# Kernel tuning notes

Hardware: AMD Instinct MI355X
Metric: run time of the kernel (lower is better)

The kernel has to match this reference:

```python
import jax, jax.numpy as jnp
import numpy as np

N_NODES = 100000
N_EDGES = 1600000
N_GRAPHS = 1024
IN_G, HID_G = 64, 128
IN_T, H1, H2 = 200, 256, 128
CONCAT = 2 * HID_G + H2  # 384


def setup_inputs() -> dict:
    key = jax.random.key(0)
    ks = jax.random.split(key, 24)
    def lin(k, fin, fout):
        kw, kb = jax.random.split(k)
        s = 1.0 / np.sqrt(fin)
        return (jax.random.uniform(kw, (fin, fout), jnp.float32, -s, s),
                jax.random.uniform(kb, (fout,), jnp.float32, -s, s))
    Wg1, bg1 = lin(ks[0], IN_G, HID_G)
    Wg2, bg2 = lin(ks[1], HID_G, HID_G)
    Wg3, bg3 = lin(ks[2], HID_G, HID_G)
    Wg4, bg4 = lin(ks[3], HID_G, HID_G)
    Wt1, bt1 = lin(ks[4], IN_T, H1)
    Wt2, bt2 = lin(ks[5], H1, H2)
    Wf1, bf1 = lin(ks[6], CONCAT, H1)
    Wf2, bf2 = lin(ks[7], H1, H2)
    Wf3, bf3 = lin(ks[8], H2, 1)
    x_graph = jax.random.normal(ks[9], (N_NODES, IN_G), jnp.float32)
    edge_index = jax.random.randint(ks[10], (2, N_EDGES), 0, N_NODES, jnp.int32)
    batch = jnp.sort(jax.random.randint(ks[11], (N_NODES,), 0, N_GRAPHS, jnp.int32))
    x_tabular = jax.random.normal(ks[12], (N_GRAPHS, IN_T), jnp.float32)
    return {"x_graph": x_graph, "edge_index": edge_index, "batch": batch,
            "x_tabular": x_tabular,
            "Wg1": Wg1, "bg1": bg1, "Wg2": Wg2, "bg2": bg2,
            "Wg3": Wg3, "bg3": bg3, "Wg4": Wg4, "bg4": bg4,
            "Wt1": Wt1, "bt1": bt1, "Wt2": Wt2, "bt2": bt2,
            "Wf1": Wf1, "bf1": bf1, "Wf2": Wf2, "bf2": bf2,
            "Wf3": Wf3, "bf3": bf3}


def _gcn(x, src, dst, norm, W, b, n):
    # x' = D^-1/2 A_hat D^-1/2 (x W) + b, scatter-add over edges
    h = x @ W
    msg = h[src] * norm[:, None]
    return jax.ops.segment_sum(msg, dst, num_segments=n) + b


def reference(x_graph, edge_index, batch, x_tabular,
              Wg1, bg1, Wg2, bg2, Wg3, bg3, Wg4, bg4,
              Wt1, bt1, Wt2, bt2, Wf1, bf1, Wf2, bf2, Wf3, bf3):
    n = x_graph.shape[0]
    b = x_tabular.shape[0]
    ar = jnp.arange(n, dtype=edge_index.dtype)
    # self-loops added once in Multi_Modal.forward + once inside GCNConv (default)
    src = jnp.concatenate([edge_index[0], ar, ar])
    dst = jnp.concatenate([edge_index[1], ar, ar])
    deg = jax.ops.segment_sum(jnp.ones(src.shape, x_graph.dtype), dst, num_segments=n)
    dinv = jnp.where(deg > 0, jax.lax.rsqrt(deg), 0.0)
    norm = dinv[src] * dinv[dst]
    h = jax.nn.relu(_gcn(x_graph, src, dst, norm, Wg1, bg1, n))
    h = jax.nn.relu(_gcn(h, src, dst, norm, Wg2, bg2, n))
    h = jax.nn.relu(_gcn(h, src, dst, norm, Wg3, bg3, n))
    h = jax.nn.relu(_gcn(h, src, dst, norm, Wg4, bg4, n))
    # global mean/max pool per graph
    cnt = jax.ops.segment_sum(jnp.ones((n,), h.dtype), batch, num_segments=b)
    mean = jax.ops.segment_sum(h, batch, num_segments=b) / jnp.maximum(cnt, 1.0)[:, None]
    mx = jax.ops.segment_max(h, batch, num_segments=b)
    x1 = jnp.concatenate([mean, mx], axis=1)
    # tabular branch
    x2 = jax.nn.relu(jax.nn.relu(x_tabular @ Wt1 + bt1) @ Wt2 + bt2)
    # fused head
    x = jnp.concatenate([x1, x2], axis=1)
    x = jax.nn.relu(x @ Wf1 + bf1)
    x = jax.nn.relu(x @ Wf2 + bf2)
    return jax.nn.sigmoid(x @ Wf3 + bf3)
```

## Files before the change

### kernel.cpp

```cpp
#include <hip/hip_runtime.h>
#include <hip/hip_bf16.h>
#include <math.h>

#define N_NODES  100000
#define N_EDGES  1600000
#define N_GRAPHS 1024

typedef __hip_bfloat16 bf16;
typedef unsigned short u16;
typedef unsigned int   u32;
typedef __attribute__((ext_vector_type(8))) short bf8_t;
typedef __attribute__((ext_vector_type(4))) float f4_t;

__device__ __forceinline__ float b2f(bf16 v) { return __bfloat162float(v); }
__device__ __forceinline__ u16 bfbits(float f) {
    bf16 h = __float2bfloat16(f);
    return *reinterpret_cast<u16*>(&h);
}
__device__ __forceinline__ float lo_bf(u32 u) { return __uint_as_float(u << 16); }
__device__ __forceinline__ float hi_bf(u32 u) { return __uint_as_float(u & 0xffff0000u); }

__global__ void sniff_init(const u16* __restrict__ xg, int* __restrict__ flag,
                           int* __restrict__ degi) {
    int i = blockIdx.x * 256 + threadIdx.x;
    if (i < N_NODES) degi[i] = 2;
    if (blockIdx.x == 0 && threadIdx.x == 0) {
        int bad = 0;
        for (int k = 0; k < 256; ++k) {
            float f = __uint_as_float(((u32)xg[k]) << 16);
            if (!(fabsf(f) < 100.f)) bad++;
        }
        *flag = (bad == 0) ? 1 : 0;
    }
}

#define NT 19
struct WTask { const void* src; void* dst; int n; int mode; };
struct PrepArgs { WTask t[NT]; int bstart[NT]; };

__global__ void prep_k(PrepArgs args, const int* __restrict__ flag) {
    int b = blockIdx.x, ti = 0;
    while (ti < NT - 1 && b >= args.bstart[ti + 1]) ++ti;
    int idx = (b - args.bstart[ti]) * 256 + threadIdx.x;
    WTask tk = args.t[ti];
    if (idx >= tk.n) return;
    int isb = *flag;
    if (tk.mode == 0) {
        float v = isb ? b2f(((const bf16*)tk.src)[idx]) : ((const float*)tk.src)[idx];
        ((float*)tk.dst)[idx] = v;
    } else if (tk.mode == 1) {
        int bseg = idx >> 9, r = idx & 511;
        int L = r >> 3, j = r & 7;
        int kb = bseg >> 3, tt = bseg & 7;
        int k = kb * 32 + ((L >> 4) << 3) + j;
        int n = (tt << 4) + (L & 15);
        int so = k * 128 + n;
        float v = isb ? b2f(((const bf16*)tk.src)[so]) : ((const float*)tk.src)[so];
        ((u16*)tk.dst)[idx] = bfbits(v);
    } else {
        u16 v = isb ? ((const u16*)tk.src)[idx] : bfbits(((const float*)tk.src)[idx]);
        ((u16*)tk.dst)[idx] = v;
    }
}

__global__ void deg_edges(const int* __restrict__ dst, int* __restrict__ degi) {
    int e = blockIdx.x * blockDim.x + threadIdx.x;
    if (e < N_EDGES) atomicAdd(&degi[dst[e]], 1);
}

#define SCAN_B 256
__global__ void scan1(const int* __restrict__ degi, int* __restrict__ ex,
                      int* __restrict__ bsum, float* __restrict__ dinv) {
    __shared__ int s[SCAN_B];
    int i = blockIdx.x * SCAN_B + threadIdx.x;
    int dg = (i < N_NODES) ? degi[i] : 2;
    int v = dg - 2;
    s[threadIdx.x] = v;
    __syncthreads();
    for (int off = 1; off < SCAN_B; off <<= 1) {
        int t = (threadIdx.x >= off) ? s[threadIdx.x - off] : 0;
        __syncthreads();
        if (threadIdx.x >= off) s[threadIdx.x] += t;
        __syncthreads();
    }
    if (i < N_NODES) {
        ex[i] = s[threadIdx.x] - v;
        dinv[i] = rsqrtf((float)dg);
    }
    if (threadIdx.x == SCAN_B - 1) bsum[blockIdx.x] = s[SCAN_B - 1];
}

__global__ void scan2(int* __restrict__ bsum, int nb) {
    __shared__ int s[512];
    int i = threadIdx.x;
    int v = (i < nb) ? bsum[i] : 0;
    s[i] = v;
    __syncthreads();
    for (int off = 1; off < 512; off <<= 1) {
        int t = (i >= off) ? s[i - off] : 0;
        __syncthreads();
        if (i >= off) s[i] += t;
        __syncthreads();
    }
    if (i < nb) bsum[i] = s[i] - v;
}

__global__ void scan3(int* __restrict__ rowptr, const int* __restrict__ bsum,
                      int* __restrict__ cnt) {
    int i = blockIdx.x * SCAN_B + threadIdx.x;
    if (i >= N_NODES) return;
    rowptr[i] += bsum[blockIdx.x];
    cnt[i] = 0;
}

__global__ void fill_csr(const int* __restrict__ src, const int* __restrict__ dst,
                         const float* __restrict__ dinv, const int* __restrict__ rowptr,
                         int* __restrict__ cnt, u32* __restrict__ csr4) {
    int e = blockIdx.x * 256 + threadIdx.x;
    if (e >= N_EDGES) return;
    int s = src[e], d = dst[e];
    int pos = rowptr[d] + atomicAdd(&cnt[d], 1);
    u32 q = (u32)__float2int_rn(dinv[s] * 32767.f);
    csr4[pos] = (q << 17) | (u32)s;
}

template<int K, bool EPI>
__global__ __launch_bounds__(256) void gemm_mfma(const u16* __restrict__ A,
        const u16* __restrict__ Wm, const float* __restrict__ bias,
        u16* __restrict__ Out, int M)
{
    int wave = threadIdx.x >> 6, lane = threadIdx.x & 63;
    int rowBase = blockIdx.x * 64 + wave * 16;
    int quad = lane >> 4, low = lane & 15;
    int arow = rowBase + low;
    if (arow >= M) arow = M - 1;
    const u16* ap = A + (size_t)arow * K + quad * 8;

    f4_t acc[8];
#pragma unroll
    for (int t = 0; t < 8; ++t) acc[t] = (f4_t)(0.f);

#pragma unroll
    for (int kb = 0; kb < K / 32; ++kb) {
        bf8_t a = *(const bf8_t*)(ap + kb * 32);
#pragma unroll
        for (int t = 0; t < 8; ++t) {
            bf8_t b = *(const bf8_t*)(Wm + (((kb << 3) + t) << 9) + lane * 8);
            acc[t] = __builtin_amdgcn_mfma_f32_16x16x32_bf16(a, b, acc[t], 0, 0, 0);
        }
    }

    int orow0 = rowBase + quad * 4;
#pragma unroll
    for (int t = 0; t < 8; ++t) {
        float bn = EPI ? bias[t * 16 + low] : 0.f;
#pragma unroll
        for (int j = 0; j < 4; ++j) {
            int r = orow0 + j;
            float v = acc[t][j];
            if (EPI) v = fmaxf(v + bn, 0.f);
            if (r < M) Out[(size_t)r * 128 + t * 16 + low] = bfbits(v);
        }
    }
}

__global__ __launch_bounds__(256) void gather_agg(
        const int* __restrict__ rowptr, const int* __restrict__ cnt,
        const u32* __restrict__ csr4, const u16* __restrict__ H,
        const float* __restrict__ dinv, const float* __restrict__ bias,
        u16* __restrict__ A)
{
    int node = blockIdx.x * 4 + (threadIdx.x >> 6);
    if (node >= N_NODES) return;
    int lane = threadIdx.x & 63;
    const u32* H2 = (const u32*)H;
    float2 bb = ((const float2*)bias)[lane];
    float dv = dinv[node];
    u32 h0 = H2[(size_t)node * 64 + lane];
    float accx = 2.f * dv * lo_bf(h0);
    float accy = 2.f * dv * hi_bf(h0);
    int p = rowptr[node];
    int end = p + cnt[node];
    const float qs = 1.f / 32767.f;
    for (; p + 8 <= end; p += 8) {
        u32 m0 = csr4[p],     m1 = csr4[p + 1];
        u32 m2 = csr4[p + 2], m3 = csr4[p + 3];
        u32 m4 = csr4[p + 4], m5 = csr4[p + 5];
        u32 m6 = csr4[p + 6], m7 = csr4[p + 7];
        u32 v0 = H2[(size_t)(m0 & 0x1FFFFu) * 64 + lane];
        u32 v1 = H2[(size_t)(m1 & 0x1FFFFu) * 64 + lane];
        u32 v2 = H2[(size_t)(m2 & 0x1FFFFu) * 64 + lane];
        u32 v3 = H2[(size_t)(m3 & 0x1FFFFu) * 64 + lane];
        u32 v4 = H2[(size_t)(m4 & 0x1FFFFu) * 64 + lane];
        u32 v5 = H2[(size_t)(m5 & 0x1FFFFu) * 64 + lane];
        u32 v6 = H2[(size_t)(m6 & 0x1FFFFu) * 64 + lane];
        u32 v7 = H2[(size_t)(m7 & 0x1FFFFu) * 64 + lane];
        float w0 = (float)(m0 >> 17) * qs, w1 = (float)(m1 >> 17) * qs;
        float w2 = (float)(m2 >> 17) * qs, w3 = (float)(m3 >> 17) * qs;
        float w4 = (float)(m4 >> 17) * qs, w5 = (float)(m5 >> 17) * qs;
        float w6 = (float)(m6 >> 17) * qs, w7 = (float)(m7 >> 17) * qs;
        accx += w0 * lo_bf(v0) + w1 * lo_bf(v1) + w2 * lo_bf(v2) + w3 * lo_bf(v3)
              + w4 * lo_bf(v4) + w5 * lo_bf(v5) + w6 * lo_bf(v6) + w7 * lo_bf(v7);
        accy += w0 * hi_bf(v0) + w1 * hi_bf(v1) + w2 * hi_bf(v2) + w3 * hi_bf(v3)
              + w4 * hi_bf(v4) + w5 * hi_bf(v5) + w6 * hi_bf(v6) + w7 * hi_bf(v7);
    }
    for (; p < end; ++p) {
        u32 m = csr4[p];
        u32 v = H2[(size_t)(m & 0x1FFFFu) * 64 + lane];
        float w = (float)(m >> 17) * qs;
        accx += w * lo_bf(v); accy += w * hi_bf(v);
    }
    accx = fmaxf(accx * dv + bb.x, 0.f);
    accy = fmaxf(accy * dv + bb.y, 0.f);
    u32 pack = ((u32)bfbits(accy) << 16) | (u32)bfbits(accx);
    ((u32*)A)[(size_t)node * 64 + lane] = pack;
}

__global__ __launch_bounds__(256) void gather_x(
        const int* __restrict__ rowptr, const int* __restrict__ cnt,
        const u32* __restrict__ csr4, const u16* __restrict__ X,
        const float* __restrict__ dinv, u16* __restrict__ G)
{
    int node = blockIdx.x * 4 + (threadIdx.x >> 6);
    if (node >= N_NODES) return;
    int lane = threadIdx.x & 63;
    int half = lane >> 5, fi = lane & 31;
    const u32* X2 = (const u32*)X;
    float dv = dinv[node];
    float accx = 0.f, accy = 0.f;
    if (half == 0) {
        u32 h0 = X2[(size_t)node * 32 + fi];
        accx = 2.f * dv * lo_bf(h0); accy = 2.f * dv * hi_bf(h0);
    }
    int rp = rowptr[node];
    int end = rp + cnt[node];
    const float qs = 1.f / 32767.f;
    int p = rp + half;
    for (; p + 6 < end; p += 8) {
        u32 m0 = csr4[p],     m1 = csr4[p + 2];
        u32 m2 = csr4[p + 4], m3 = csr4[p + 6];
        u32 v0 = X2[(size_t)(m0 & 0x1FFFFu) * 32 + fi];
        u32 v1 = X2[(size_t)(m1 & 0x1FFFFu) * 32 + fi];
        u32 v2 = X2[(size_t)(m2 & 0x1FFFFu) * 32 + fi];
        u32 v3 = X2[(size_t)(m3 & 0x1FFFFu) * 32 + fi];
        float w0 = (float)(m0 >> 17) * qs, w1 = (float)(m1 >> 17) * qs;
        float w2 = (float)(m2 >> 17) * qs, w3 = (float)(m3 >> 17) * qs;
        accx += w0 * lo_bf(v0) + w1 * lo_bf(v1) + w2 * lo_bf(v2) + w3 * lo_bf(v3);
        accy += w0 * hi_bf(v0) + w1 * hi_bf(v1) + w2 * hi_bf(v2) + w3 * hi_bf(v3);
    }
    for (; p < end; p += 2) {
        u32 m = csr4[p];
        u32 v = X2[(size_t)(m & 0x1FFFFu) * 32 + fi];
        float w = (float)(m >> 17) * qs;
        accx += w * lo_bf(v); accy += w * hi_bf(v);
    }
    accx += __shfl_xor(accx, 32);
    accy += __shfl_xor(accy, 32);
    if (half == 0) {
        accx *= dv; accy *= dv;
        u32 pack = ((u32)bfbits(accy) << 16) | (u32)bfbits(accx);
        ((u32*)G)[(size_t)node * 32 + fi] = pack;
    }
}

__global__ __launch_bounds__(256) void tail_k(const u16* __restrict__ A,
        const int* __restrict__ batch, const void* __restrict__ x_tab,
        const float* __restrict__ Wt1, const float* __restrict__ bt1,
        const float* __restrict__ Wt2, const float* __restrict__ bt2,
        const float* __restrict__ Wf1, const float* __restrict__ bf1,
        const float* __restrict__ Wf2, const float* __restrict__ bf2,
        const float* __restrict__ Wf3, const float* __restrict__ bf3,
        void* __restrict__ out, const int* __restrict__ flagp)
{
    __shared__ float xs[384];
    __shared__ float t1s[256];
    __shared__ float u1s[256];
    __shared__ float u2s[128];
    __shared__ float xts[200];
    __shared__ float ps[256], pm[256];
    __shared__ int sb[2];
    int g = blockIdx.x;
    int tid = threadIdx.x;
    if (tid == 0) {
        int lo = 0, hi = N_NODES;
        while (lo < hi) { int m = (lo + hi) >> 1; if (batch[m] < g) lo = m + 1; else hi = m; }
        sb[0] = lo;
        hi = N_NODES;
        while (lo < hi) { int m = (lo + hi) >> 1; if (batch[m] < g + 1) lo = m + 1; else hi = m; }
        sb[1] = lo;
    }
    int isb = *flagp;
    if (tid < 200)
        xts[tid] = isb ? b2f(((const bf16*)x_tab)[(size_t)g * 200 + tid])
                       : ((const float*)x_tab)[(size_t)g * 200 + tid];
    __syncthreads();
    int start = sb[0], end = sb[1];
    int t = tid & 127, half = tid >> 7;
    float sum = 0.f, mx = -3.4e38f;
    for (int n = start + half; n < end; n += 2) {
        float v = __uint_as_float(((u32)A[(size_t)n * 128 + t]) << 16);
        sum += v; mx = fmaxf(mx, v);
    }
    ps[tid] = sum; pm[tid] = mx;
    __syncthreads();
    if (half == 0) {
        int c = end - start;
        float s2 = ps[t] + ps[t + 128];
        float m2 = fmaxf(pm[t], pm[t + 128]);
        xs[t] = s2 / (float)(c > 0 ? c : 1);
        xs[128 + t] = (c > 0) ? m2 : 0.f;
    }
    float acc = bt1[tid];
    for (int k = 0; k < 200; ++k) acc += xts[k] * Wt1[k * 256 + tid];
    t1s[tid] = fmaxf(acc, 0.f);
    __syncthreads();
    if (tid < 128) {
        acc = bt2[tid];
        for (int k = 0; k < 256; ++k) acc += t1s[k] * Wt2[k * 128 + tid];
        xs[256 + tid] = fmaxf(acc, 0.f);
    }
    __syncthreads();
    acc = bf1[tid];
    for (int k = 0; k < 384; ++k) acc += xs[k] * Wf1[k * 256 + tid];
    u1s[tid] = fmaxf(acc, 0.f);
    __syncthreads();
    if (tid < 128) {
        acc = bf2[tid];
        for (int k = 0; k < 256; ++k) acc += u1s[k] * Wf2[k * 128 + tid];
        u2s[tid] = fmaxf(acc, 0.f);
    }
    __syncthreads();
    if (tid < 64) {
        float a = u2s[tid] * Wf3[tid] + u2s[tid + 64] * Wf3[tid + 64];
        for (int off = 32; off > 0; off >>= 1) a += __shfl_down(a, off);
        if (tid == 0) {
            float z = a + bf3[0];
            float sg = 1.f / (1.f + expf(-z));
            if (isb) ((bf16*)out)[g] = __float2bfloat16(sg);
            else     ((float*)out)[g] = sg;
        }
    }
}

extern "C" void kernel_launch(void* const* d_in, const int* in_sizes, int n_in,
                              void* d_out, int out_size, void* d_ws, size_t ws_size,
                              hipStream_t stream) {
    const void* x_graph    = d_in[0];
    const int*  edge_index = (const int*)d_in[1];
    const int*  batch      = (const int*)d_in[2];
    const void* x_tab      = d_in[3];

    const int* src  = edge_index;
    const int* dstp = edge_index + N_EDGES;

    char* wsp = (char*)d_ws;
    int*  flag = (int*)wsp;                      wsp += 16;
    u16*  A16  = (u16*)wsp;                      wsp += (size_t)N_NODES * 128 * 2;
    u16*  B16  = (u16*)wsp;                      wsp += (size_t)N_NODES * 128 * 2;
    u16*  X16  = (u16*)wsp;                      wsp += (size_t)N_NODES * 64 * 2;
    u16*  G16  = (u16*)wsp;                      wsp += (size_t)N_NODES * 64 * 2;
    u16*  Wm[4];
    Wm[0] = (u16*)wsp;                           wsp += 64 * 128 * 2;
    Wm[1] = (u16*)wsp;                           wsp += 128 * 128 * 2;
    Wm[2] = (u16*)wsp;                           wsp += 128 * 128 * 2;
    Wm[3] = (u16*)wsp;                           wsp += 128 * 128 * 2;
    float* p = (float*)wsp;
    float* bg1f = p; p += 128;
    float* bg2f = p; p += 128;
    float* bg3f = p; p += 128;
    float* bg4f = p; p += 128;
    float* Wt1f = p; p += 200 * 256; float* bt1f = p; p += 256;
    float* Wt2f = p; p += 256 * 128; float* bt2f = p; p += 128;
    float* Wf1f = p; p += 384 * 256; float* bf1f = p; p += 256;
    float* Wf2f = p; p += 256 * 128; float* bf2f = p; p += 128;
    float* Wf3f = p; p += 128;       float* bf3f = p; p += 4;
    int*   degi   = (int*)p;            p += N_NODES;
    float* dinv   = p;                  p += N_NODES;
    int*   rowptr = (int*)p;            p += N_NODES;
    int*   cnt    = (int*)p;            p += N_NODES;
    int*   bsum   = (int*)p;            p += 512;
    u32*   csr4   = (u32*)p;            p += N_EDGES;

    sniff_init<<<(N_NODES + 255) / 256, 256, 0, stream>>>((const u16*)x_graph, flag, degi);

    PrepArgs pa;
    auto setT = [&](int i, const void* s, void* d, int n, int mode) {
        pa.t[i].src = s; pa.t[i].dst = d; pa.t[i].n = n; pa.t[i].mode = mode;
    };
    setT(0,  d_in[4],  Wm[0], 64 * 128, 1);
    setT(1,  d_in[6],  Wm[1], 128 * 128, 1);
    setT(2,  d_in[8],  Wm[2], 128 * 128, 1);
    setT(3,  d_in[10], Wm[3], 128 * 128, 1);
    setT(4,  d_in[12], Wt1f, 200 * 256, 0);
    setT(5,  d_in[14], Wt2f, 256 * 128, 0);
    setT(6,  d_in[16], Wf1f, 384 * 256, 0);
    setT(7,  d_in[18], Wf2f, 256 * 128, 0);
    setT(8,  d_in[20], Wf3f, 128, 0);
    setT(9,  d_in[5],  bg1f, 128, 0);
    setT(10, d_in[7],  bg2f, 128, 0);
    setT(11, d_in[9],  bg3f, 128, 0);
    setT(12, d_in[11], bg4f, 128, 0);
    setT(13, d_in[13], bt1f, 256, 0);
    setT(14, d_in[15], bt2f, 128, 0);
    setT(15, d_in[17], bf1f, 256, 0);
    setT(16, d_in[19], bf2f, 128, 0);
    setT(17, d_in[21], bf3f, 1, 0);
    setT(18, d_in[0],  X16, N_NODES * 64, 2);
    int totalBlocks = 0;
    for (int i = 0; i < NT; ++i) {
        pa.bstart[i] = totalBlocks;
        totalBlocks += (pa.t[i].n + 255) / 256;
    }
    prep_k<<<totalBlocks, 256, 0, stream>>>(pa, flag);

    const int nb = (N_NODES + SCAN_B - 1) / SCAN_B;
    deg_edges<<<(N_EDGES + 255) / 256, 256, 0, stream>>>(dstp, degi);
    scan1<<<nb, SCAN_B, 0, stream>>>(degi, rowptr, bsum, dinv);
    scan2<<<1, 512, 0, stream>>>(bsum, nb);
    scan3<<<nb, SCAN_B, 0, stream>>>(rowptr, bsum, cnt);
    fill_csr<<<(N_EDGES + 255) / 256, 256, 0, stream>>>(src, dstp, dinv, rowptr, cnt, csr4);

    const int gemmGrid = (N_NODES + 63) / 64;
    const int aggGrid  = (N_NODES + 3) / 4;

    gather_x<<<aggGrid, 256, 0, stream>>>(rowptr, cnt, csr4, X16, dinv, G16);
    gemm_mfma<64, true><<<gemmGrid, 256, 0, stream>>>(G16, Wm[0], bg1f, A16, N_NODES);

    const float* bgL[4] = {bg1f, bg2f, bg3f, bg4f};
    for (int l = 1; l < 4; ++l) {
        gemm_mfma<128, false><<<gemmGrid, 256, 0, stream>>>(A16, Wm[l], nullptr, B16, N_NODES);
        gather_agg<<<aggGrid, 256, 0, stream>>>(rowptr, cnt, csr4, B16, dinv, bgL[l], A16);
    }

    tail_k<<<N_GRAPHS, 256, 0, stream>>>(A16, batch, x_tab,
        Wt1f, bt1f, Wt2f, bt2f, Wf1f, bf1f, Wf2f, bf2f, Wf3f, bf3f, d_out, flag);
}
```

Measured before the change: 733.4 us.

## Build CSR via two-level bucket sort with padded per-bucket slabs

Replaces the global-atomic degree count, three-pass scan and per-edge atomic CSR fill with a bucketed counting sort. Edges are first binned by destination into 391 buckets of 256 nodes using shared-memory histograms. Each bucket then computes local degrees, row pointers, dinv and quantized dinv, and scatters the entries into a padded slab using shared-memory atomics. This cuts contended global atomics and kernel launches, but relies on a fixed pad of 5120 edges per bucket, which could overflow on skewed graphs. The CSR layout becomes non-contiguous, with rowptr offsets based on bucket*BPAD.

```diff
diff --git a/kernel.cpp b/kernel.cpp
--- a/kernel.cpp
+++ b/kernel.cpp
@@ -5,6 +5,8 @@
 #define N_NODES  100000
 #define N_EDGES  1600000
 #define N_GRAPHS 1024
+#define NBUCK    391
+#define BPAD     5120
 
 typedef __hip_bfloat16 bf16;
 typedef unsigned short u16;
@@ -20,11 +22,11 @@
 __device__ __forceinline__ float lo_bf(u32 u) { return __uint_as_float(u << 16); }
 __device__ __forceinline__ float hi_bf(u32 u) { return __uint_as_float(u & 0xffff0000u); }
 
-__global__ void sniff_init(const u16* __restrict__ xg, int* __restrict__ flag,
-                           int* __restrict__ degi) {
-    int i = blockIdx.x * 256 + threadIdx.x;
-    if (i < N_NODES) degi[i] = 2;
-    if (blockIdx.x == 0 && threadIdx.x == 0) {
+__global__ void sniff_k(const u16* __restrict__ xg, int* __restrict__ flag,
+                        int* __restrict__ gbucket) {
+    int tid = threadIdx.x;
+    if (tid < NBUCK) gbucket[tid] = 0;
+    if (tid == 511) {
         int bad = 0;
         for (int k = 0; k < 256; ++k) {
             float f = __uint_as_float(((u32)xg[k]) << 16);
@@ -63,65 +65,86 @@
     }
 }
 
-__global__ void deg_edges(const int* __restrict__ dst, int* __restrict__ degi) {
-    int e = blockIdx.x * blockDim.x + threadIdx.x;
-    if (e < N_EDGES) atomicAdd(&degi[dst[e]], 1);
-}
-
-#define SCAN_B 256
-__global__ void scan1(const int* __restrict__ degi, int* __restrict__ ex,
-                      int* __restrict__ bsum, float* __restrict__ dinv) {
-    __shared__ int s[SCAN_B];
-    int i = blockIdx.x * SCAN_B + threadIdx.x;
-    int dg = (i < N_NODES) ? degi[i] : 2;
-    int v = dg - 2;
-    s[threadIdx.x] = v;
-    __syncthreads();
-    for (int off = 1; off < SCAN_B; off <<= 1) {
-        int t = (threadIdx.x >= off) ? s[threadIdx.x - off] : 0;
+#define BIN_CH 4093
+__global__ __launch_bounds__(256) void bin_a(const int* __restrict__ src,
+        const int* __restrict__ dst, int* __restrict__ gbucket,
+        u32* __restrict__ st) {
+    __shared__ int hist[NBUCK];
+    __shared__ int bas[NBUCK];
+    int b = blockIdx.x, tid = threadIdx.x;
+    for (int j = tid; j < NBUCK; j += 256) hist[j] = 0;
+    __syncthreads();
+    int e0 = b * BIN_CH;
+    int eend = e0 + BIN_CH; if (eend > N_EDGES) eend = N_EDGES;
+    for (int e = e0 + tid; e < eend; e += 256)
+        atomicAdd(&hist[dst[e] >> 8], 1);
+    __syncthreads();
+    for (int j = tid; j < NBUCK; j += 256) {
+        int c = hist[j];
+        bas[j] = c ? atomicAdd(&gbucket[j], c) : 0;
+        hist[j] = 0;
+    }
+    __syncthreads();
+    for (int e = e0 + tid; e < eend; e += 256) {
+        int d = dst[e], s = src[e];
+        int bk = d >> 8;
+        int idx = atomicAdd(&hist[bk], 1);
+        st[(size_t)bk * BPAD + bas[bk] + idx] = ((u32)(d & 255) << 17) | (u32)s;
+    }
+}
+
+__global__ __launch_bounds__(256) void b1_nodes(const int* __restrict__ gbucket,
+        const u32* __restrict__ st, int* __restrict__ rowptr,
+        int* __restrict__ cnt, float* __restrict__ dinv, u16* __restrict__ qd) {
+    __shared__ int nh[256];
+    __shared__ int s[256];
+    int b = blockIdx.x, tid = threadIdx.x;
+    nh[tid] = 0;
+    __syncthreads();
+    int cb = gbucket[b];
+    const u32* stb = st + (size_t)b * BPAD;
+    for (int i = tid; i < cb; i += 256)
+        atomicAdd(&nh[(stb[i] >> 17) & 255], 1);
+    __syncthreads();
+    int own = nh[tid];
+    s[tid] = own;
+    __syncthreads();
+    for (int off = 1; off < 256; off <<= 1) {
+        int t = (tid >= off) ? s[tid - off] : 0;
         __syncthreads();
-        if (threadIdx.x >= off) s[threadIdx.x] += t;
+        if (tid >= off) s[tid] += t;
         __syncthreads();
     }
-    if (i < N_NODES) {
-        ex[i] = s[threadIdx.x] - v;
-        dinv[i] = rsqrtf((float)dg);
-    }
-    if (threadIdx.x == SCAN_B - 1) bsum[blockIdx.x] = s[SCAN_B - 1];
-}
-
-__global__ void scan2(int* __restrict__ bsum, int nb) {
-    __shared__ int s[512];
-    int i = threadIdx.x;
-    int v = (i < nb) ? bsum[i] : 0;
-    s[i] = v;
-    __syncthreads();
-    for (int off = 1; off < 512; off <<= 1) {
-        int t = (i >= off) ? s[i - off] : 0;
-        __syncthreads();
-        if (i >= off) s[i] += t;
-        __syncthreads();
-    }
-    if (i < nb) bsum[i] = s[i] - v;
-}
-
-__global__ void scan3(int* __restrict__ rowptr, const int* __restrict__ bsum,
-                      int* __restrict__ cnt) {
-    int i = blockIdx.x * SCAN_B + threadIdx.x;
-    if (i >= N_NODES) return;
-    rowptr[i] += bsum[blockIdx.x];
-    cnt[i] = 0;
-}
-
-__global__ void fill_csr(const int* __restrict__ src, const int* __restrict__ dst,
-                         const float* __restrict__ dinv, const int* __restrict__ rowptr,
-                         int* __restrict__ cnt, u32* __restrict__ csr4) {
-    int e = blockIdx.x * 256 + threadIdx.x;
-    if (e >= N_EDGES) return;
-    int s = src[e], d = dst[e];
-    int pos = rowptr[d] + atomicAdd(&cnt[d], 1);
-    u32 q = (u32)__float2int_rn(dinv[s] * 32767.f);
-    csr4[pos] = (q << 17) | (u32)s;
+    int ex = s[tid] - own;
+    int n = b * 256 + tid;
+    if (n < N_NODES) {
+        rowptr[n] = b * BPAD + ex;
+        cnt[n] = own;
+        float dv = rsqrtf((float)(own + 2));
+        dinv[n] = dv;
+        qd[n] = (u16)__float2int_rn(dv * 32767.f);
+    }
+}
+
+__global__ __launch_bounds__(256) void b2_scatter(const int* __restrict__ gbucket,
+        const u32* __restrict__ st, const int* __restrict__ rowptr,
+        const u16* __restrict__ qd, u32* __restrict__ csr4) {
+    __shared__ int rp[256];
+    __shared__ int lc[256];
+    int b = blockIdx.x, tid = threadIdx.x;
+    int n = b * 256 + tid;
+    rp[tid] = (n < N_NODES) ? rowptr[n] : 0;
+    lc[tid] = 0;
+    __syncthreads();
+    int cb = gbucket[b];
+    const u32* stb = st + (size_t)b * BPAD;
+    for (int i = tid; i < cb; i += 256) {
+        u32 v = stb[i];
+        int ld = (v >> 17) & 255;
+        u32 sidx = v & 0x1FFFFu;
+        int idx = atomicAdd(&lc[ld], 1);
+        csr4[rp[ld] + idx] = ((u32)qd[sidx] << 17) | sidx;
+    }
 }
 
 template<int K, bool EPI>
@@ -374,14 +397,15 @@
     float* Wf1f = p; p += 384 * 256; float* bf1f = p; p += 256;
     float* Wf2f = p; p += 256 * 128; float* bf2f = p; p += 128;
     float* Wf3f = p; p += 128;       float* bf3f = p; p += 4;
-    int*   degi   = (int*)p;            p += N_NODES;
     float* dinv   = p;                  p += N_NODES;
     int*   rowptr = (int*)p;            p += N_NODES;
     int*   cnt    = (int*)p;            p += N_NODES;
-    int*   bsum   = (int*)p;            p += 512;
-    u32*   csr4   = (u32*)p;            p += N_EDGES;
-
-    sniff_init<<<(N_NODES + 255) / 256, 256, 0, stream>>>((const u16*)x_graph, flag, degi);
+    u16*   qd     = (u16*)p;            p += (N_NODES + 1) / 2;
+    int*   gbucket= (int*)p;            p += 512;
+    u32*   st     = (u32*)p;            p += (size_t)NBUCK * BPAD;
+    u32*   csr4   = (u32*)p;            p += (size_t)NBUCK * BPAD;
+
+    sniff_k<<<1, 512, 0, stream>>>((const u16*)x_graph, flag, gbucket);
 
     PrepArgs pa;
     auto setT = [&](int i, const void* s, void* d, int n, int mode) {
@@ -413,12 +437,9 @@
     }
     prep_k<<<totalBlocks, 256, 0, stream>>>(pa, flag);
 
-    const int nb = (N_NODES + SCAN_B - 1) / SCAN_B;
-    deg_edges<<<(N_EDGES + 255) / 256, 256, 0, stream>>>(dstp, degi);
-    scan1<<<nb, SCAN_B, 0, stream>>>(degi, rowptr, bsum, dinv);
-    scan2<<<1, 512, 0, stream>>>(bsum, nb);
-    scan3<<<nb, SCAN_B, 0, stream>>>(rowptr, bsum, cnt);
-    fill_csr<<<(N_EDGES + 255) / 256, 256, 0, stream>>>(src, dstp, dinv, rowptr, cnt, csr4);
+    bin_a<<<NBUCK, 256, 0, stream>>>(src, dstp, gbucket, st);
+    b1_nodes<<<NBUCK, 256, 0, stream>>>(gbucket, st, rowptr, cnt, dinv, qd);
+    b2_scatter<<<NBUCK, 256, 0, stream>>>(gbucket, st, rowptr, qd, csr4);
 
     const int gemmGrid = (N_NODES + 63) / 64;
     const int aggGrid  = (N_NODES + 3) / 4;
```

New measurement: 628.2 us. 1.17x faster.
